# Kernel optimization log

Measured on AMD Instinct MI355X. Metric: run time of the kernel, lower is better.

The kernel has to match this reference:

```python
import jax, jax.numpy as jnp
import numpy as np

BS = 16   # block_size
SR = 16   # search_range


def setup_inputs() -> dict:
    key = jax.random.key(0)
    k1, k2 = jax.random.split(key)
    H, W = 2048, 2048
    current_frame = jax.random.uniform(k1, (H, W), dtype=jnp.float32)
    reference_frame = jax.random.uniform(k2, (H, W), dtype=jnp.float32)
    return {"current_frame": current_frame, "reference_frame": reference_frame}


def reference(current_frame, reference_frame):
    H, W = current_frame.shape
    bs, sr = BS, SR
    nby, nbx = H // bs, W // bs
    # zero-pad reference by search_range on all sides (matches F.pad constant 0)
    ref_p = jnp.pad(reference_frame, sr)
    # offsets in the same iteration order as the torch loops: dy outer, dx inner
    d = jnp.arange(-sr, sr + 1, dtype=jnp.int32)
    offs = jnp.stack(jnp.meshgrid(d, d, indexing="ij"), axis=-1).reshape(-1, 2)  # [(2sr+1)^2, 2]

    init = (
        jnp.full((nby, nbx), jnp.inf, dtype=jnp.float32),   # min_sad
        jnp.zeros((nby, nbx), dtype=jnp.float32),            # motion_x
        jnp.zeros((nby, nbx), dtype=jnp.float32),            # motion_y
    )

    def step(carry, off):
        best_sad, mx, my = carry
        dy, dx = off[0], off[1]
        # shifted reference plane: ref_padded[sr+dy : sr+dy+H, sr+dx : sr+dx+W]
        ref_shift = jax.lax.dynamic_slice(ref_p, (sr + dy, sr + dx), (H, W))
        # per-block SAD: sum |cur - ref| over each bs x bs tile
        sad = jnp.abs(current_frame - ref_shift).reshape(nby, bs, nbx, bs).sum(axis=(1, 3))
        better = sad < best_sad
        new_carry = (
            jnp.where(better, sad, best_sad),
            jnp.where(better, dx.astype(jnp.float32), mx),
            jnp.where(better, dy.astype(jnp.float32), my),
        )
        return new_carry, None

    (min_sad, motion_x, motion_y), _ = jax.lax.scan(step, init, offs)
    return motion_x, motion_y, min_sad
```

## Files before the change

### kernel.cpp

```cpp
#include <hip/hip_runtime.h>


#define HH 2048
#define WW 2048
#define NB 128
#define RSTR 164
#define CSTR 128
#define SCALE 16777216.0f
#define INV_SCALE 5.9604644775390625e-08f

__device__ __forceinline__ void sadacc(unsigned a, unsigned b, unsigned& c) {
    asm("v_sad_u32 %0, %1, %2, %0" : "+v"(c) : "v"(a), "v"(b));
}

__launch_bounds__(512, 6)
__global__ void me_kernel(const float* __restrict__ cur,
                          const float* __restrict__ ref,
                          float* __restrict__ out) {
    __shared__ __align__(16) unsigned lds_ref[48 * RSTR];
    __shared__ __align__(16) unsigned lds_cur[16 * CSTR];

    const int tid = threadIdx.x;
    const int wg  = blockIdx.x;
    const int by  = wg >> 4;
    const int bx0 = (wg & 15) << 3;

    const int gy0 = by * 16 - 16;
    const int gx0 = bx0 * 16 - 16;
#pragma unroll
    for (int k = 0; k < 15; ++k) {
        int i = tid + k * 512;
        int r = i / 160;
        int c = i - r * 160;
        int gy = gy0 + r, gx = gx0 + c;
        float v = 0.f;
        if (gy >= 0 && gy < HH && gx >= 0 && gx < WW) v = ref[gy * WW + gx];
        lds_ref[r * RSTR + c] = (unsigned)(v * SCALE);
    }
#pragma unroll
    for (int k = 0; k < 4; ++k) {
        int i = tid + k * 512;
        int r = i >> 7, c = i & 127;
        lds_cur[i] = (unsigned)(cur[(by * 16 + r) * WW + bx0 * 16 + c] * SCALE);
    }
    __syncthreads();

    const int l  = tid & 63;
    const int b  = tid >> 6;
    const int n  = l >> 1;
    const int m  = l & 1;
    const int cb = b * 16;

    unsigned acc[16];
#pragma unroll
    for (int d = 0; d < 16; ++d) acc[d] = 0u;
    unsigned eacc = 0u;

    const unsigned* refbase = &lds_ref[n * RSTR + cb + 16 * m];
    const unsigned* curbase = &lds_cur[cb];
    const unsigned* ep = (l < 33) ? &lds_ref[l * RSTR + cb + 32]
                                  : &lds_ref[32 * RSTR + cb + (l - 33)];

#pragma unroll 4
    for (int y = 0; y < 16; ++y) {
        unsigned cu[16];
#pragma unroll
        for (int q = 0; q < 4; ++q) {
            uint4 v = *(const uint4*)&curbase[y * CSTR + 4 * q];
            cu[4*q+0] = v.x; cu[4*q+1] = v.y; cu[4*q+2] = v.z; cu[4*q+3] = v.w;
        }
        unsigned eb[16];
        if (l < 33) {
#pragma unroll
            for (int q = 0; q < 4; ++q) {
                uint4 v = *(const uint4*)&ep[y * RSTR + 4 * q];
                eb[4*q+0] = v.x; eb[4*q+1] = v.y; eb[4*q+2] = v.z; eb[4*q+3] = v.w;
            }
        } else {
#pragma unroll
            for (int x = 0; x < 16; ++x) eb[x] = ep[y * RSTR + x];
        }
#pragma unroll
        for (int x = 0; x < 16; ++x) sadacc(cu[x], eb[x], eacc);
#pragma unroll
        for (int q = 0; q < 8; ++q) {
            uint4 v = *(const uint4*)&refbase[y * RSTR + 4 * q];
            unsigned vv[4] = {v.x, v.y, v.z, v.w};
#pragma unroll
            for (int j = 0; j < 4; ++j) {
                const int s = 4 * q + j;
                if (s <= 30) {
                    const int lo = s > 15 ? s - 15 : 0;
                    const int hi = s < 15 ? s : 15;
#pragma unroll
                    for (int dd = lo; dd <= hi; ++dd)
                        sadacc(cu[s - dd], vv[j], acc[dd]);
                }
            }
        }
    }

    unsigned long long best = ~0ull;
#pragma unroll
    for (int dd = 0; dd < 16; ++dd) {
        unsigned long long p =
            ((unsigned long long)acc[dd] << 32) | (unsigned)(n * 33 + 16 * m + dd);
        best = p < best ? p : best;
    }
    {
        unsigned eidx = (l < 33) ? (unsigned)(l * 33 + 32) : (unsigned)(32 * 33 + (l - 33));
        unsigned long long p = ((unsigned long long)eacc << 32) | eidx;
        best = p < best ? p : best;
    }
    {
        int r = l >> 2, c0 = (l & 3) * 4;
        unsigned s = 0u;
#pragma unroll
        for (int c = 0; c < 4; ++c)
            sadacc(lds_cur[r * CSTR + cb + c0 + c],
                   lds_ref[(32 + r) * RSTR + cb + 31 + c0 + c], s);
#pragma unroll
        for (int sh = 32; sh > 0; sh >>= 1) s += __shfl_xor(s, sh, 64);
        unsigned long long p = ((unsigned long long)s << 32) | 1087u;
        best = p < best ? p : best;
    }
#pragma unroll
    for (int sh = 32; sh > 0; sh >>= 1) {
        unsigned long long o = __shfl_xor(best, sh, 64);
        best = o < best ? o : best;
    }
    if (l == 0) {
        unsigned idx  = (unsigned)(best & 0xffffffffu);
        unsigned sadu = (unsigned)(best >> 32);
        int dy = (int)(idx / 33) - 16;
        int dx = (int)(idx % 33) - 16;
        int bi = by * NB + (bx0 + b);
        out[bi]             = (float)dx;
        out[16384 + bi]     = (float)dy;
        out[2 * 16384 + bi] = (float)sadu * INV_SCALE;
    }
}

extern "C" void kernel_launch(void* const* d_in, const int* in_sizes, int n_in,
                              void* d_out, int out_size, void* d_ws, size_t ws_size,
                              hipStream_t stream) {
    const float* cur = (const float*)d_in[0];
    const float* ref = (const float*)d_in[1];
    float* out = (float*)d_out;
    (void)in_sizes; (void)n_in; (void)out_size; (void)d_ws; (void)ws_size;
    me_kernel<<<dim3(2048), dim3(512), 0, stream>>>(cur, ref, out);
}
```

Baseline: 205.6 us.

## Process two tiles per workgroup, prefetching the second tile during first compute

Each workgroup now handles two consecutive tiles with double-buffered LDS. The global loads for the second tile are issued into registers before computing the first tile, then written to the second LDS buffer, so memory latency overlaps with SAD compute. Grid size is halved and launch bounds are lowered to 4 waves-per-EU hints. The cost is doubled LDS per workgroup and extra live registers for the staged values, which lowers occupancy, along with fewer workgroups to balance across CUs.

```diff
diff --git a/kernel.cpp b/kernel.cpp
--- a/kernel.cpp
+++ b/kernel.cpp
@@ -13,18 +13,11 @@
     asm("v_sad_u32 %0, %1, %2, %0" : "+v"(c) : "v"(a), "v"(b));
 }
 
-__launch_bounds__(512, 6)
-__global__ void me_kernel(const float* __restrict__ cur,
-                          const float* __restrict__ ref,
-                          float* __restrict__ out) {
-    __shared__ __align__(16) unsigned lds_ref[48 * RSTR];
-    __shared__ __align__(16) unsigned lds_cur[16 * CSTR];
+struct StageRegs { float rr[15]; float rc[4]; };
 
-    const int tid = threadIdx.x;
-    const int wg  = blockIdx.x;
-    const int by  = wg >> 4;
-    const int bx0 = (wg & 15) << 3;
-
+__device__ __forceinline__ void stage_load(const float* __restrict__ cur,
+                                           const float* __restrict__ ref,
+                                           int by, int bx0, int tid, StageRegs& s) {
     const int gy0 = by * 16 - 16;
     const int gx0 = bx0 * 16 - 16;
 #pragma unroll
@@ -33,20 +26,36 @@
         int r = i / 160;
         int c = i - r * 160;
         int gy = gy0 + r, gx = gx0 + c;
-        float v = 0.f;
-        if (gy >= 0 && gy < HH && gx >= 0 && gx < WW) v = ref[gy * WW + gx];
-        lds_ref[r * RSTR + c] = (unsigned)(v * SCALE);
+        s.rr[k] = (gy >= 0 && gy < HH && gx >= 0 && gx < WW) ? ref[gy * WW + gx] : 0.f;
     }
 #pragma unroll
     for (int k = 0; k < 4; ++k) {
         int i = tid + k * 512;
         int r = i >> 7, c = i & 127;
-        lds_cur[i] = (unsigned)(cur[(by * 16 + r) * WW + bx0 * 16 + c] * SCALE);
+        s.rc[k] = cur[(by * 16 + r) * WW + bx0 * 16 + c];
     }
-    __syncthreads();
+}
 
-    const int l  = tid & 63;
-    const int b  = tid >> 6;
+__device__ __forceinline__ void stage_write(unsigned* lref, unsigned* lcur,
+                                            int tid, const StageRegs& s) {
+#pragma unroll
+    for (int k = 0; k < 15; ++k) {
+        int i = tid + k * 512;
+        int r = i / 160;
+        int c = i - r * 160;
+        lref[r * RSTR + c] = (unsigned)(s.rr[k] * SCALE);
+    }
+#pragma unroll
+    for (int k = 0; k < 4; ++k) {
+        int i = tid + k * 512;
+        lcur[i] = (unsigned)(s.rc[k] * SCALE);
+    }
+}
+
+__device__ __forceinline__ void compute_tile(const unsigned* __restrict__ lref,
+                                             const unsigned* __restrict__ lcur,
+                                             int by, int bx0, int l, int b,
+                                             float* __restrict__ out) {
     const int n  = l >> 1;
     const int m  = l & 1;
     const int cb = b * 16;
@@ -56,10 +65,10 @@
     for (int d = 0; d < 16; ++d) acc[d] = 0u;
     unsigned eacc = 0u;
 
-    const unsigned* refbase = &lds_ref[n * RSTR + cb + 16 * m];
-    const unsigned* curbase = &lds_cur[cb];
-    const unsigned* ep = (l < 33) ? &lds_ref[l * RSTR + cb + 32]
-                                  : &lds_ref[32 * RSTR + cb + (l - 33)];
+    const unsigned* refbase = &lref[n * RSTR + cb + 16 * m];
+    const unsigned* curbase = &lcur[cb];
+    const unsigned* ep = (l < 33) ? &lref[l * RSTR + cb + 32]
+                                  : &lref[32 * RSTR + cb + (l - 33)];
 
 #pragma unroll 4
     for (int y = 0; y < 16; ++y) {
@@ -117,8 +126,8 @@
         unsigned s = 0u;
 #pragma unroll
         for (int c = 0; c < 4; ++c)
-            sadacc(lds_cur[r * CSTR + cb + c0 + c],
-                   lds_ref[(32 + r) * RSTR + cb + 31 + c0 + c], s);
+            sadacc(lcur[r * CSTR + cb + c0 + c],
+                   lref[(32 + r) * RSTR + cb + 31 + c0 + c], s);
 #pragma unroll
         for (int sh = 32; sh > 0; sh >>= 1) s += __shfl_xor(s, sh, 64);
         unsigned long long p = ((unsigned long long)s << 32) | 1087u;
@@ -141,6 +150,39 @@
     }
 }
 
+__launch_bounds__(512, 4)
+__global__ void me_kernel(const float* __restrict__ cur,
+                          const float* __restrict__ ref,
+                          float* __restrict__ out) {
+    __shared__ __align__(16) unsigned lref0[48 * RSTR];
+    __shared__ __align__(16) unsigned lcur0[16 * CSTR];
+    __shared__ __align__(16) unsigned lref1[48 * RSTR];
+    __shared__ __align__(16) unsigned lcur1[16 * CSTR];
+
+    const int tid = threadIdx.x;
+    const int l   = tid & 63;
+    const int b   = tid >> 6;
+    const int g0  = 2 * blockIdx.x;
+    const int g1  = g0 + 1;
+    const int by0 = g0 >> 4, bx00 = (g0 & 15) << 3;
+    const int by1 = g1 >> 4, bx01 = (g1 & 15) << 3;
+
+    StageRegs s;
+    stage_load(cur, ref, by0, bx00, tid, s);
+    stage_write(lref0, lcur0, tid, s);
+    __syncthreads();
+
+    stage_load(cur, ref, by1, bx01, tid, s);
+    __builtin_amdgcn_sched_barrier(0);
+
+    compute_tile(lref0, lcur0, by0, bx00, l, b, out);
+
+    stage_write(lref1, lcur1, tid, s);
+    __syncthreads();
+
+    compute_tile(lref1, lcur1, by1, bx01, l, b, out);
+}
+
 extern "C" void kernel_launch(void* const* d_in, const int* in_sizes, int n_in,
                               void* d_out, int out_size, void* d_ws, size_t ws_size,
                               hipStream_t stream) {
@@ -148,5 +190,5 @@
     const float* ref = (const float*)d_in[1];
     float* out = (float*)d_out;
     (void)in_sizes; (void)n_in; (void)out_size; (void)d_ws; (void)ws_size;
-    me_kernel<<<dim3(2048), dim3(512), 0, stream>>>(cur, ref, out);
+    me_kernel<<<dim3(1024), dim3(512), 0, stream>>>(cur, ref, out);
 }
```

Result: slower. 220.3 us (+7.1%).

## Split reference staging in two phases to overlap tail loads with SAD compute

Applied to the files above, without the earlier changes.

The kernel now stages only the first 40 rows of the reference window into LDS before computing. The last 8 rows are prefetched into registers and kept in flight through the first 8 rows of SAD work, then written to LDS behind a second barrier before the remaining rows are processed. Interior tiles get a bounds-check-free load path, and the occupancy hint in launch bounds is lowered from 6 to 4. The aim is to hide global load latency behind compute, at the cost of an extra barrier, more register pressure and a duplicated code body.

```diff
diff --git a/kernel.cpp b/kernel.cpp
--- a/kernel.cpp
+++ b/kernel.cpp
@@ -13,12 +13,12 @@
     asm("v_sad_u32 %0, %1, %2, %0" : "+v"(c) : "v"(a), "v"(b));
 }
 
-__launch_bounds__(512, 6)
+__launch_bounds__(512, 4)
 __global__ void me_kernel(const float* __restrict__ cur,
                           const float* __restrict__ ref,
                           float* __restrict__ out) {
-    __shared__ __align__(16) unsigned lds_ref[48 * RSTR];
-    __shared__ __align__(16) unsigned lds_cur[16 * CSTR];
+    __shared__ __align__(16) unsigned lref[48 * RSTR];
+    __shared__ __align__(16) unsigned lcur[16 * CSTR];
 
     const int tid = threadIdx.x;
     const int wg  = blockIdx.x;
@@ -27,23 +27,62 @@
 
     const int gy0 = by * 16 - 16;
     const int gx0 = bx0 * 16 - 16;
-#pragma unroll
-    for (int k = 0; k < 15; ++k) {
-        int i = tid + k * 512;
-        int r = i / 160;
-        int c = i - r * 160;
-        int gy = gy0 + r, gx = gx0 + c;
-        float v = 0.f;
-        if (gy >= 0 && gy < HH && gx >= 0 && gx < WW) v = ref[gy * WW + gx];
-        lds_ref[r * RSTR + c] = (unsigned)(v * SCALE);
+    const bool interior = (by > 0) & (by < 127) & (bx0 > 0) & (bx0 < 120);
+
+    if (interior) {
+#pragma unroll
+        for (int k = 0; k < 13; ++k) {
+            int i = tid + k * 512;
+            if (k < 12 || i < 6400) {
+                int r = i / 160, c = i - r * 160;
+                lref[r * RSTR + c] = (unsigned)(ref[(gy0 + r) * WW + gx0 + c] * SCALE);
+            }
+        }
+    } else {
+#pragma unroll
+        for (int k = 0; k < 13; ++k) {
+            int i = tid + k * 512;
+            if (k < 12 || i < 6400) {
+                int r = i / 160, c = i - r * 160;
+                int gy = gy0 + r, gx = gx0 + c;
+                float v = 0.f;
+                if (gy >= 0 && gy < HH && gx >= 0 && gx < WW) v = ref[gy * WW + gx];
+                lref[r * RSTR + c] = (unsigned)(v * SCALE);
+            }
+        }
     }
 #pragma unroll
     for (int k = 0; k < 4; ++k) {
         int i = tid + k * 512;
         int r = i >> 7, c = i & 127;
-        lds_cur[i] = (unsigned)(cur[(by * 16 + r) * WW + bx0 * 16 + c] * SCALE);
+        lcur[i] = (unsigned)(cur[(by * 16 + r) * WW + bx0 * 16 + c] * SCALE);
     }
     __syncthreads();
+
+    float br[3];
+    {
+        if (interior) {
+#pragma unroll
+            for (int k = 0; k < 3; ++k) {
+                int i = tid + k * 512;
+                if (k < 2 || i < 1280) {
+                    int r = 40 + (i / 160), c = (i % 160);
+                    br[k] = ref[(gy0 + r) * WW + gx0 + c];
+                }
+            }
+        } else {
+#pragma unroll
+            for (int k = 0; k < 3; ++k) {
+                int i = tid + k * 512;
+                if (k < 2 || i < 1280) {
+                    int r = 40 + (i / 160), c = (i % 160);
+                    int gy = gy0 + r, gx = gx0 + c;
+                    br[k] = (gy >= 0 && gy < HH && gx >= 0 && gx < WW) ? ref[gy * WW + gx] : 0.f;
+                }
+            }
+        }
+    }
+    __builtin_amdgcn_sched_barrier(0);
 
     const int l  = tid & 63;
     const int b  = tid >> 6;
@@ -56,13 +95,13 @@
     for (int d = 0; d < 16; ++d) acc[d] = 0u;
     unsigned eacc = 0u;
 
-    const unsigned* refbase = &lds_ref[n * RSTR + cb + 16 * m];
-    const unsigned* curbase = &lds_cur[cb];
-    const unsigned* ep = (l < 33) ? &lds_ref[l * RSTR + cb + 32]
-                                  : &lds_ref[32 * RSTR + cb + (l - 33)];
+    const unsigned* refbase = &lref[n * RSTR + cb + 16 * m];
+    const unsigned* curbase = &lcur[cb];
+    const unsigned* ep = (l < 33) ? &lref[l * RSTR + cb + 32]
+                                  : &lref[32 * RSTR + cb + (l - 33)];
 
 #pragma unroll 4
-    for (int y = 0; y < 16; ++y) {
+    for (int y = 0; y < 8; ++y) {
         unsigned cu[16];
 #pragma unroll
         for (int q = 0; q < 4; ++q) {
@@ -100,6 +139,55 @@
         }
     }
 
+#pragma unroll
+    for (int k = 0; k < 3; ++k) {
+        int i = tid + k * 512;
+        if (k < 2 || i < 1280) {
+            int r = 40 + (i / 160), c = (i % 160);
+            lref[r * RSTR + c] = (unsigned)(br[k] * SCALE);
+        }
+    }
+    __syncthreads();
+
+#pragma unroll 4
+    for (int y = 8; y < 16; ++y) {
+        unsigned cu[16];
+#pragma unroll
+        for (int q = 0; q < 4; ++q) {
+            uint4 v = *(const uint4*)&curbase[y * CSTR + 4 * q];
+            cu[4*q+0] = v.x; cu[4*q+1] = v.y; cu[4*q+2] = v.z; cu[4*q+3] = v.w;
+        }
+        unsigned eb[16];
+        if (l < 33) {
+#pragma unroll
+            for (int q = 0; q < 4; ++q) {
+                uint4 v = *(const uint4*)&ep[y * RSTR + 4 * q];
+                eb[4*q+0] = v.x; eb[4*q+1] = v.y; eb[4*q+2] = v.z; eb[4*q+3] = v.w;
+            }
+        } else {
+#pragma unroll
+            for (int x = 0; x < 16; ++x) eb[x] = ep[y * RSTR + x];
+        }
+#pragma unroll
+        for (int x = 0; x < 16; ++x) sadacc(cu[x], eb[x], eacc);
+#pragma unroll
+        for (int q = 0; q < 8; ++q) {
+            uint4 v = *(const uint4*)&refbase[y * RSTR + 4 * q];
+            unsigned vv[4] = {v.x, v.y, v.z, v.w};
+#pragma unroll
+            for (int j = 0; j < 4; ++j) {
+                const int s = 4 * q + j;
+                if (s <= 30) {
+                    const int lo = s > 15 ? s - 15 : 0;
+                    const int hi = s < 15 ? s : 15;
+#pragma unroll
+                    for (int dd = lo; dd <= hi; ++dd)
+                        sadacc(cu[s - dd], vv[j], acc[dd]);
+                }
+            }
+        }
+    }
+
     unsigned long long best = ~0ull;
 #pragma unroll
     for (int dd = 0; dd < 16; ++dd) {
@@ -117,8 +205,8 @@
         unsigned s = 0u;
 #pragma unroll
         for (int c = 0; c < 4; ++c)
-            sadacc(lds_cur[r * CSTR + cb + c0 + c],
-                   lds_ref[(32 + r) * RSTR + cb + 31 + c0 + c], s);
+            sadacc(lcur[r * CSTR + cb + c0 + c],
+                   lref[(32 + r) * RSTR + cb + 31 + c0 + c], s);
 #pragma unroll
         for (int sh = 32; sh > 0; sh >>= 1) s += __shfl_xor(s, sh, 64);
         unsigned long long p = ((unsigned long long)s << 32) | 1087u;
```

Result: no change. 207.5 us (+0.9%).
